# Kernel optimization log

Measured on AMD Instinct MI355X. Metric: run time of the kernel, lower is better.

The kernel has to match this reference:

```python
import jax, jax.numpy as jnp
import numpy as np

NQ = 4096
N0, N1 = 32768, 8192
N = N0 + N1
F = 128          # emb_dim (32x0e+32x1e)
H = 4            # num_heads
HD = F // H
NB = 64          # fc_neurons[0] radial basis size
DEG = 32
CUTOFFS = jnp.array([2.0, 4.0], dtype=jnp.float32)
OFFSETS = jnp.array([0.1, 0.2], dtype=jnp.float32)


def _sph_harm(u):
    # component-normalized real spherical harmonics l=0,1,2 of unit vectors u [E,3]
    x, y, z = u[:, 0], u[:, 1], u[:, 2]
    s3, s15, s5 = 3.0 ** 0.5, 15.0 ** 0.5, 5.0 ** 0.5
    return jnp.stack([
        jnp.ones_like(x),
        s3 * x, s3 * y, s3 * z,
        s15 * x * y, s15 * y * z, 0.5 * s5 * (3.0 * z * z - 1.0),
        s15 * x * z, 0.5 * s15 * (x * x - y * y),
    ], axis=-1)  # [E,9]


def setup_inputs() -> dict:
    key = jax.random.key(0)
    ks = jax.random.split(key, 20)
    E0 = NQ * DEG
    E1 = NQ * DEG
    edge_src = jnp.concatenate([
        jax.random.randint(ks[0], (E0,), 0, N0),
        jax.random.randint(ks[1], (E1,), N0, N),
    ])
    edge_dst = jnp.concatenate([
        jax.random.randint(ks[2], (E0,), 0, NQ),
        jax.random.randint(ks[3], (E1,), 0, NQ),
    ])
    scale_id = jnp.concatenate([jnp.zeros((E0,), jnp.int32), jnp.ones((E1,), jnp.int32)])
    r = lambda k, sh, s=1.0: jax.random.normal(k, sh, jnp.float32) * s
    return {
        'query_coord': r(ks[4], (NQ, 3)),
        'node_feature': r(ks[5], (N, F)),
        'node_coord': r(ks[6], (N, 3)),
        'edge_src': edge_src, 'edge_dst': edge_dst, 'scale_id': scale_id,
        'b_dst': r(ks[7], (F,)),
        'Wq': r(ks[8], (F, F), F ** -0.5),
        'Wk': r(ks[9], (F, F), F ** -0.5),
        'Wv': r(ks[10], (F, F), F ** -0.5),
        'Wo': r(ks[11], (F, F), F ** -0.5),
        'bo': r(ks[12], (F,)),
        'W_rad0': r(ks[13], (NB, NB), NB ** -0.5), 'b_rad0': r(ks[14], (NB,)),
        'W_rad1': r(ks[15], (NB, NB), NB ** -0.5), 'b_rad1': r(ks[16], (NB,)),
        'W_msg': r(ks[17], (NB, F), NB ** -0.5),
        'W_sh': r(ks[18], (9, F), 9 ** -0.5),
        'W_alpha': r(ks[19], (NB, H), NB ** -0.5),
    }


def _forward(query_coord, node_feature, node_coord, b_dst, Wq, Wk, Wv, Wo, bo,
             W_rad0, b_rad0, W_rad1, b_rad1, W_msg, W_sh, W_alpha,
             edge_src, edge_dst, scale_id):
    Nq = query_coord.shape[0]
    vec = node_coord[edge_src] - query_coord[edge_dst]            # [E,3]
    rlen = jnp.sqrt(jnp.sum(vec * vec, -1) + 1e-12)               # [E]
    off = OFFSETS[scale_id]
    cut = CUTOFFS[scale_id]
    xn = (rlen - off) / (cut - off)                               # normalized radius per scale
    centers = jnp.linspace(0.0, 1.0, NB)
    std = 1.0 / NB
    g = jnp.exp(-0.5 * ((xn[:, None] - centers) / std) ** 2)      # [E,NB] gaussian RBF
    soft = 0.5 * (1.0 + jnp.cos(jnp.pi * jnp.clip((xn - 0.8) / 0.2, 0.0, 1.0)))
    g = g * soft[:, None]                                         # soft finite cutoff
    # per-scale Linear after radial basis (2 scales, masked select)
    edge_scalar = jnp.where((scale_id == 0)[:, None], g @ W_rad0 + b_rad0, g @ W_rad1 + b_rad1)
    sh = _sph_harm(vec / rlen[:, None])                           # [E,9]
    # attention GNN (equiformer-style): dst features start as zeros + learned bias
    q = (b_dst @ Wq).reshape(H, HD)
    k = (node_feature @ Wk)[edge_src].reshape(-1, H, HD)
    logits = jnp.einsum('hd,ehd->eh', q, k) / (HD ** 0.5) + edge_scalar @ W_alpha  # [E,H]
    m = jax.ops.segment_max(logits, edge_dst, num_segments=Nq)
    p = jnp.exp(logits - m[edge_dst])
    denom = jax.ops.segment_sum(p, edge_dst, num_segments=Nq)
    alpha = p / (denom[edge_dst] + 1e-9)                          # segment softmax [E,H]
    v_e = (node_feature @ Wv)[edge_src] * (edge_scalar @ W_msg) + sh @ W_sh  # [E,F]
    msg = (alpha[:, :, None] * v_e.reshape(-1, H, HD)).reshape(-1, F)
    out = jax.ops.segment_sum(msg, edge_dst, num_segments=Nq)     # [Nq,F]
    return out @ Wo + bo


def reference(query_coord, node_feature, node_coord, edge_src, edge_dst, scale_id,
              b_dst, Wq, Wk, Wv, Wo, bo, W_rad0, b_rad0, W_rad1, b_rad1,
              W_msg, W_sh, W_alpha):
    return _forward(query_coord, node_feature, node_coord, b_dst, Wq, Wk, Wv, Wo, bo,
                    W_rad0, b_rad0, W_rad1, b_rad1, W_msg, W_sh, W_alpha,
                    edge_src, edge_dst, scale_id)
```

## Files before the change

### kernel.cpp

```cpp
#include <hip/hip_runtime.h>
#include <hip/hip_bf16.h>
#include <math.h>

#define PI_F 3.14159265358979323846f

typedef __attribute__((ext_vector_type(8))) short short8v;
typedef __attribute__((ext_vector_type(4))) float f32x4;

__device__ __forceinline__ short f2bf(float x) {
    return __builtin_bit_cast(short, __float2bfloat16(x));
}
__device__ __forceinline__ float bf2f(unsigned short u) {
    return __uint_as_float(((unsigned)u) << 16);
}
__device__ __forceinline__ int pack_bf2(float a, float b) {
    return (int)(unsigned short)f2bf(a) | ((int)(unsigned short)f2bf(b) << 16);
}

static const size_t WS_WA     = 0;
static const size_t WS_BA     = 512;
static const size_t WS_BM     = 520;
static const size_t WS_WMF    = 776;
static const size_t WS_WSHF   = 8968;
static const size_t WS_QKF    = 11016;
static const size_t WS_WVF    = 12040;
static const size_t WS_WOF    = 20232;
static const size_t WS_COUNTS = 28424;
static const size_t WS_OFFS   = 36624;
static const size_t WS_CURSOR = 44824;
static const size_t WS_PACKED = 53016;
static const size_t WS_LK     = 315160;
static const size_t WS_EDP    = 479000;
static const size_t WS_EDG    = 1527576;
static const size_t WS_VB     = 2576152;
static const size_t WS_OUTPRE = 5197592;

__global__ __launch_bounds__(256) void k_prepfmt(
    const float* b_dst, const float* Wq, const float* Wk,
    const float* W_rad0, const float* b_rad0,
    const float* W_rad1, const float* b_rad1,
    const float* W_msg, const float* W_alpha, const float* Wv,
    const float* Wo, const float* W_sh,
    float* Wa, float* ba, float* bm,
    short* WmF, short* WshF, short* QKF, short* WVF, short* WOF,
    int* counts, int nkey) {
    __shared__ float qs_s[128];
    __shared__ float qk_s[512];
    int t = threadIdx.x;
    int b = blockIdx.x;
    if (b == 0) {
        if (t < 128) {
            float acc = 0.f;
            for (int c = 0; c < 128; ++c) acc += b_dst[c] * Wq[c * 128 + t];
            qs_s[t] = acc;
        }
        __syncthreads();
        if (t < 128) {
            const float invs = 0.17677669529663687f;
            for (int h = 0; h < 4; ++h) {
                float acc = 0.f;
                for (int d = 0; d < 32; ++d)
                    acc += Wk[t * 128 + h * 32 + d] * qs_s[h * 32 + d];
                qk_s[t * 4 + h] = acc * invs;
            }
        }
        for (int idx = t; idx < 512; idx += 256) {
            int s = idx >> 8, i = (idx >> 2) & 63, h = idx & 3;
            const float* Wr = s ? W_rad1 : W_rad0;
            float acc = 0.f;
            for (int u = 0; u < 64; ++u) acc += Wr[i * 64 + u] * W_alpha[u * 4 + h];
            Wa[idx] = acc;
        }
        if (t < 8) {
            int s = t >> 2, h = t & 3;
            const float* br = s ? b_rad1 : b_rad0;
            float acc = 0.f;
            for (int u = 0; u < 64; ++u) acc += br[u] * W_alpha[u * 4 + h];
            ba[t] = acc;
        }
        {
            int s = t >> 7, c = t & 127;
            const float* br = s ? b_rad1 : b_rad0;
            float acc = 0.f;
            for (int u = 0; u < 64; ++u) acc += br[u] * W_msg[u * 128 + c];
            bm[t] = acc;
        }
        __syncthreads();
        for (int idx = t; idx < 2048; idx += 256) {
            int j = idx & 7, lane = (idx >> 3) & 63, kh = idx >> 9;
            int k = kh * 32 + ((lane >> 4) << 3) + j;
            int col = lane & 15;
            QKF[idx] = f2bf(col < 4 ? qk_s[k * 4 + col] : 0.f);
        }
    } else if (b <= 208) {
        int item = (b - 1) * 256 + t;
        if (item < 16384) {
            int j = item & 7, lane = (item >> 3) & 63, kh = (item >> 9) & 1;
            int ct = (item >> 10) & 7, sid = item >> 13;
            int k = kh * 32 + ((lane >> 4) << 3) + j;
            int c = (lane & 15) * 8 + ct;
            const float* Wr = sid ? W_rad1 : W_rad0;
            float acc = 0.f;
            for (int u = 0; u < 64; ++u) acc += Wr[k * 64 + u] * W_msg[u * 128 + c];
            WmF[item] = f2bf(acc);
        } else if (item < 20480) {
            int i2 = item - 16384;
            int j = i2 & 7, lane = (i2 >> 3) & 63, ct = (i2 >> 9) & 7;
            int k = ((lane >> 4) << 3) + j;
            int c = (lane & 15) * 8 + ct;
            WshF[i2] = f2bf(k < 9 ? W_sh[k * 128 + c] : 0.f);
        } else if (item < 36864) {
            int i2 = item - 20480;
            int j = i2 & 7, lane = (i2 >> 3) & 63, ct = (i2 >> 9) & 7, kh = (i2 >> 12) & 3;
            int k = kh * 32 + ((lane >> 4) << 3) + j;
            int c = (lane & 15) * 8 + ct;
            WVF[i2] = f2bf(Wv[k * 128 + c]);
        } else {
            int i2 = item - 36864;
            int j = i2 & 7, lane = (i2 >> 3) & 63, ct = (i2 >> 9) & 7, kh = (i2 >> 12) & 3;
            int k = kh * 32 + ((lane >> 4) << 3) + j;
            int c = (lane & 15) * 8 + ct;
            WOF[i2] = f2bf(Wo[k * 128 + c]);
        }
    } else {
        int idx = (b - 209) * 256 + t;
        if (idx < nkey) counts[idx] = 0;
    }
}

template <typename OUT, bool LK>
__global__ __launch_bounds__(256) void k_mgemm(
    const float* A, const short* WF, const float* bias, OUT* out,
    float* lk, const short* QKF, int M,
    const int* edge_dst, const int* scale_id, int* counts, int E, int NQr) {
    int gb = (M + 63) >> 6;
    if ((int)blockIdx.x >= gb) {
        int e = ((int)blockIdx.x - gb) * 256 + (int)threadIdx.x;
        if (e < E) atomicAdd(&counts[scale_id[e] * NQr + edge_dst[e]], 1);
        return;
    }
    int t = threadIdx.x;
    int w = t >> 6, lane = t & 63;
    int m = lane & 15, grp = lane >> 4;
    int row0 = (blockIdx.x * 4 + w) * 16;
    if (row0 >= M) return;

    short8v a[4];
#pragma unroll
    for (int kh = 0; kh < 4; ++kh) {
        const float* ap = &A[(size_t)(row0 + m) * 128 + kh * 32 + grp * 8];
        float4 f0 = *(const float4*)ap;
        float4 f1 = *(const float4*)(ap + 4);
        a[kh][0] = f2bf(f0.x); a[kh][1] = f2bf(f0.y);
        a[kh][2] = f2bf(f0.z); a[kh][3] = f2bf(f0.w);
        a[kh][4] = f2bf(f1.x); a[kh][5] = f2bf(f1.y);
        a[kh][6] = f2bf(f1.z); a[kh][7] = f2bf(f1.w);
    }
    if constexpr (LK) {
        f32x4 cl = {0.f, 0.f, 0.f, 0.f};
#pragma unroll
        for (int kh = 0; kh < 4; ++kh) {
            short8v qb = *(const short8v*)&QKF[(kh * 64 + lane) * 8];
            cl = __builtin_amdgcn_mfma_f32_16x16x32_bf16(a[kh], qb, cl, 0, 0, 0);
        }
        if (m < 4) {
#pragma unroll
            for (int r = 0; r < 4; ++r)
                lk[(size_t)(row0 + grp * 4 + r) * 4 + m] = cl[r];
        }
    }
    f32x4 c8[8];
#pragma unroll
    for (int ct = 0; ct < 8; ++ct) {
        f32x4 c = {0.f, 0.f, 0.f, 0.f};
#pragma unroll
        for (int kh = 0; kh < 4; ++kh) {
            short8v bf = *(const short8v*)&WF[((kh * 8 + ct) * 64 + lane) * 8];
            c = __builtin_amdgcn_mfma_f32_16x16x32_bf16(a[kh], bf, c, 0, 0, 0);
        }
        c8[ct] = c;
    }
    if constexpr (sizeof(OUT) == 2) {
#pragma unroll
        for (int r = 0; r < 4; ++r) {
            int row = row0 + grp * 4 + r;
            int4 sv;
            sv.x = pack_bf2(c8[0][r], c8[1][r]);
            sv.y = pack_bf2(c8[2][r], c8[3][r]);
            sv.z = pack_bf2(c8[4][r], c8[5][r]);
            sv.w = pack_bf2(c8[6][r], c8[7][r]);
            *(int4*)&out[(size_t)row * 128 + m * 8] = sv;
        }
    } else {
        float4 b0 = make_float4(0.f, 0.f, 0.f, 0.f), b1 = b0;
        if (bias) {
            b0 = *(const float4*)&bias[m * 8];
            b1 = *(const float4*)&bias[m * 8 + 4];
        }
#pragma unroll
        for (int r = 0; r < 4; ++r) {
            int row = row0 + grp * 4 + r;
            float4 o0 = make_float4(c8[0][r] + b0.x, c8[1][r] + b0.y,
                                    c8[2][r] + b0.z, c8[3][r] + b0.w);
            float4 o1 = make_float4(c8[4][r] + b1.x, c8[5][r] + b1.y,
                                    c8[6][r] + b1.z, c8[7][r] + b1.w);
            *(float4*)&out[(size_t)row * 128 + m * 8] = o0;
            *(float4*)&out[(size_t)row * 128 + m * 8 + 4] = o1;
        }
    }
}

__global__ void k_scan(const int* counts, int* offsets, int* cursor, int nkey) {
    __shared__ int sdata[256];
    int t = threadIdx.x;
    int chunk = (nkey + 255) / 256;
    int sum = 0;
    for (int i = 0; i < chunk; ++i) {
        int idx = t * chunk + i;
        sum += (idx < nkey) ? counts[idx] : 0;
    }
    sdata[t] = sum;
    __syncthreads();
    for (int off = 1; off < 256; off <<= 1) {
        int v = (t >= off) ? sdata[t - off] : 0;
        __syncthreads();
        sdata[t] += v;
        __syncthreads();
    }
    int run = sdata[t] - sum;
    for (int i = 0; i < chunk; ++i) {
        int idx = t * chunk + i;
        if (idx < nkey) {
            offsets[idx] = run;
            cursor[idx] = run;
            run += counts[idx];
        }
    }
    if (t == 255) offsets[nkey] = sdata[255];
}

__global__ __launch_bounds__(256) void k_scatter_edge(
    const int* edge_src, const int* edge_dst, const int* scale_id,
    const float* qc, const float* nc, const float* lk,
    const float* WaB, const float* baB, int* cursor,
    int* packed, float* edP, float* edG, int E, int NQr) {
    __shared__ float WaS[512];
    __shared__ float baS[8];
    int t = threadIdx.x;
    for (int i = t; i < 512; i += 256) WaS[i] = WaB[i];
    if (t < 8) baS[t] = baB[t];
    __syncthreads();
    int e = blockIdx.x * 256 + t;
    if (e >= E) return;
    int src = edge_src[e], dst = edge_dst[e], sid = scale_id[e];
    int pos = atomicAdd(&cursor[sid * NQr + dst], 1);

    float qx = qc[dst * 3 + 0], qy = qc[dst * 3 + 1], qz = qc[dst * 3 + 2];
    float vx = nc[src * 3 + 0] - qx;
    float vy = nc[src * 3 + 1] - qy;
    float vz = nc[src * 3 + 2] - qz;
    float r = sqrtf(vx * vx + vy * vy + vz * vz + 1e-12f);
    float rinv = 1.0f / r;
    float ux = vx * rinv, uy = vy * rinv, uz = vz * rinv;

    float roff = sid ? 0.2f : 0.1f;
    float rdiv = sid ? (1.0f / 3.8f) : (1.0f / 1.9f);
    float xn = (r - roff) * rdiv;
    float su = fminf(fmaxf((xn - 0.8f) * 5.0f, 0.0f), 1.0f);
    float soft = 0.5f * (1.0f + __cosf(PI_F * su));

    float4 lkv = *(const float4*)&lk[(size_t)src * 4];

    const float qs = 64.f / 63.f;
    const float Qc = __expf(-qs * qs);
    const float* Wrow = WaS + sid * 256;
    float a0 = 0.f, a1 = 0.f, a2 = 0.f, a3 = 0.f;
#pragma unroll
    for (int ch = 0; ch < 8; ++ch) {
        float d = (xn - (float)(ch * 8) * (1.0f / 63.0f)) * 64.0f;
        float g = __expf(-0.5f * d * d);
        float tt = __expf(fminf(qs * d - 0.5f * qs * qs, 60.f));
#pragma unroll
        for (int j = 0; j < 8; ++j) {
            float4 wa = *(const float4*)&Wrow[(ch * 8 + j) * 4];
            a0 = fmaf(g, wa.x, a0);
            a1 = fmaf(g, wa.y, a1);
            a2 = fmaf(g, wa.z, a2);
            a3 = fmaf(g, wa.w, a3);
            g *= tt; tt *= Qc;
        }
    }
    float p0 = __expf(lkv.x + soft * a0 + baS[sid * 4 + 0]);
    float p1 = __expf(lkv.y + soft * a1 + baS[sid * 4 + 1]);
    float p2 = __expf(lkv.z + soft * a2 + baS[sid * 4 + 2]);
    float p3 = __expf(lkv.w + soft * a3 + baS[sid * 4 + 3]);
    packed[pos] = src | (dst << 16);
    *(float4*)&edP[(size_t)pos * 4] = make_float4(p0, p1, p2, p3);
    *(float4*)&edG[(size_t)pos * 4] = make_float4(ux, uy, uz, xn);
}

__device__ __forceinline__ short8v gchain(float xn, int k0, float soft, float Qc) {
    const float qs = 64.f / 63.f;
    float d = (xn - (float)k0 * (1.0f / 63.0f)) * 64.0f;
    float g = __expf(-0.5f * d * d);
    float tt = __expf(fminf(qs * d - 0.5f * qs * qs, 60.f));
    short8v rr;
#pragma unroll
    for (int j = 0; j < 8; ++j) {
        rr[j] = f2bf(g * soft);
        g *= tt; tt *= Qc;
    }
    return rr;
}

__global__ __launch_bounds__(256) void k_main10(
    const int* offsets, const int* packed, const float* edP, const float* edG,
    const unsigned short* Vu, const float* bm, const short* WmF, const short* WshF,
    float* out_pre, int NQr) {
    __shared__ float part[4][132];
    int t = threadIdx.x;
    int w = t >> 6, lane = t & 63;
    int sid = w & 1;
    int dst = blockIdx.x * 2 + (w >> 1);
    int m = lane & 15, grp = lane >> 4;
    int h = m >> 2;

    int key = sid * NQr + dst;
    int s0 = offsets[key], s1 = offsets[key + 1];
    int nt = (s1 - s0 + 15) >> 4;

    float acc[8];
#pragma unroll
    for (int i = 0; i < 8; ++i) acc[i] = 0.f;
    float den = 0.f;

    float4 bm0 = *(const float4*)&bm[sid * 128 + m * 8];
    float4 bm1 = *(const float4*)&bm[sid * 128 + m * 8 + 4];
    float bmv[8] = {bm0.x, bm0.y, bm0.z, bm0.w, bm1.x, bm1.y, bm1.z, bm1.w};
    const short* wmp = WmF + sid * 8192;

    const float qs = 64.f / 63.f;
    const float Qc = __expf(-qs * qs);
    const float s3 = 1.7320508075688772f, s15 = 3.872983346207417f, s5 = 2.23606797749979f;

    if (nt > 0) {
        auto loadA = [&](int tl, int (&srcs)[4], float (&ph)[4], float4& G4) {
            int q0 = s0 + tl * 16;
            int posA = q0 + m; if (posA >= s1) posA = s1 - 1;
            G4 = *(const float4*)&edG[(size_t)posA * 4];
#pragma unroll
            for (int r = 0; r < 4; ++r) {
                int pos = q0 + grp * 4 + r;
                bool valid = pos < s1;
                if (!valid) pos = s1 - 1;
                srcs[r] = packed[pos] & 0xFFFF;
                float p = edP[(size_t)pos * 4 + h];
                ph[r] = valid ? p : 0.f;
            }
        };
        auto loadV = [&](const int (&srcs)[4], int4 (&vv)[4]) {
#pragma unroll
            for (int r = 0; r < 4; ++r)
                vv[r] = *(const int4*)&Vu[(size_t)srcs[r] * 128 + m * 8];
        };

        int srcsA[4], srcsB[4], srcsC[4];
        float phA[4], phB[4], phC[4];
        float4 gA, gB, gC;
        int4 vA[4], vB[4];

        loadA(0, srcsA, phA, gA);
        loadV(srcsA, vA);
        if (nt > 1) loadA(1, srcsB, phB, gB);

        for (int tl = 0; tl < nt; ++tl) {
            if (tl + 1 < nt) loadV(srcsB, vB);
            if (tl + 2 < nt) loadA(tl + 2, srcsC, phC, gC);

            int wds[4][4];
#pragma unroll
            for (int r = 0; r < 4; ++r) {
                wds[r][0] = vA[r].x; wds[r][1] = vA[r].y;
                wds[r][2] = vA[r].z; wds[r][3] = vA[r].w;
            }
            den += phA[0] + phA[1] + phA[2] + phA[3];

            float xn = gA.w;
            float su = fminf(fmaxf((xn - 0.8f) * 5.0f, 0.0f), 1.0f);
            float soft = 0.5f * (1.0f + __cosf(PI_F * su));
            short8v aG0 = gchain(xn, grp * 8, soft, Qc);
            short8v aG1 = gchain(xn, 32 + grp * 8, soft, Qc);

            float ux = gA.x, uy = gA.y, uz = gA.z;
            float sh[9];
            sh[0] = 1.f; sh[1] = s3 * ux; sh[2] = s3 * uy; sh[3] = s3 * uz;
            sh[4] = s15 * ux * uy; sh[5] = s15 * uy * uz;
            sh[6] = 0.5f * s5 * (3.f * uz * uz - 1.f);
            sh[7] = s15 * ux * uz; sh[8] = 0.5f * s15 * (ux * ux - uy * uy);
            short8v aS;
#pragma unroll
            for (int j = 0; j < 8; ++j) {
                float v = (grp == 0) ? sh[j] : ((grp == 1 && j == 0) ? sh[8] : 0.f);
                aS[j] = f2bf(v);
            }

#pragma unroll
            for (int ct = 0; ct < 8; ++ct) {
                short8v b0 = *(const short8v*)&wmp[((ct * 2 + 0) * 64 + lane) * 8];
                short8v b1 = *(const short8v*)&wmp[((ct * 2 + 1) * 64 + lane) * 8];
                short8v bS = *(const short8v*)&WshF[(ct * 64 + lane) * 8];
                f32x4 cms = {bmv[ct], bmv[ct], bmv[ct], bmv[ct]};
                cms = __builtin_amdgcn_mfma_f32_16x16x32_bf16(aG0, b0, cms, 0, 0, 0);
                cms = __builtin_amdgcn_mfma_f32_16x16x32_bf16(aG1, b1, cms, 0, 0, 0);
                f32x4 csh = {0.f, 0.f, 0.f, 0.f};
                csh = __builtin_amdgcn_mfma_f32_16x16x32_bf16(aS, bS, csh, 0, 0, 0);
#pragma unroll
                for (int r = 0; r < 4; ++r) {
                    int wd = wds[r][ct >> 1];
                    unsigned short vu = (ct & 1) ? (unsigned short)(wd >> 16)
                                                 : (unsigned short)(wd & 0xFFFF);
                    float vf = bf2f(vu);
                    float ve = fmaf(vf, cms[r], csh[r]);
                    acc[ct] = fmaf(phA[r], ve, acc[ct]);
                }
            }

            gA = gB; gB = gC;
#pragma unroll
            for (int r = 0; r < 4; ++r) {
                phA[r] = phB[r]; phB[r] = phC[r];
                srcsB[r] = srcsC[r];
                vA[r] = vB[r];
            }
        }
    }

#pragma unroll
    for (int i = 0; i < 8; ++i) {
        acc[i] += __shfl_xor(acc[i], 16);
        acc[i] += __shfl_xor(acc[i], 32);
    }
    den += __shfl_xor(den, 16);
    den += __shfl_xor(den, 32);
    if (lane < 16) {
#pragma unroll
        for (int ct = 0; ct < 8; ++ct) part[w][m * 8 + ct] = acc[ct];
        if ((m & 3) == 0) part[w][128 + h] = den;
    }
    __syncthreads();

    {
        int which = t >> 7;
        int col = t & 127;
        int d2 = blockIdx.x * 2 + which;
        if (d2 < NQr) {
            int hh = col >> 5;
            float s = part[2 * which][col] + part[2 * which + 1][col];
            float d = part[2 * which][128 + hh] + part[2 * which + 1][128 + hh];
            out_pre[(size_t)d2 * 128 + col] = s / (d + 1e-9f);
        }
    }
}

extern "C" void kernel_launch(void* const* d_in, const int* in_sizes, int n_in,
                              void* d_out, int out_size, void* d_ws, size_t ws_size,
                              hipStream_t stream) {
    const float* query_coord = (const float*)d_in[0];
    const float* node_feature = (const float*)d_in[1];
    const float* node_coord = (const float*)d_in[2];
    const int* edge_src = (const int*)d_in[3];
    const int* edge_dst = (const int*)d_in[4];
    const int* scale_id = (const int*)d_in[5];
    const float* b_dst = (const float*)d_in[6];
    const float* Wq = (const float*)d_in[7];
    const float* Wk = (const float*)d_in[8];
    const float* Wv = (const float*)d_in[9];
    const float* Wo = (const float*)d_in[10];
    const float* bo = (const float*)d_in[11];
    const float* W_rad0 = (const float*)d_in[12];
    const float* b_rad0 = (const float*)d_in[13];
    const float* W_rad1 = (const float*)d_in[14];
    const float* b_rad1 = (const float*)d_in[15];
    const float* W_msg = (const float*)d_in[16];
    const float* W_sh = (const float*)d_in[17];
    const float* W_alpha = (const float*)d_in[18];
    (void)n_in; (void)ws_size; (void)out_size;

    int NQr = in_sizes[0] / 3;
    int Nn = in_sizes[1] / 128;
    int E = in_sizes[3];
    int nkey = NQr * 2;

    float* ws = (float*)d_ws;
    float* Wa = ws + WS_WA;
    float* ba = ws + WS_BA;
    float* bm = ws + WS_BM;
    short* WmF = (short*)(ws + WS_WMF);
    short* WshF = (short*)(ws + WS_WSHF);
    short* QKF = (short*)(ws + WS_QKF);
    short* WVF = (short*)(ws + WS_WVF);
    short* WOF = (short*)(ws + WS_WOF);
    int* counts = (int*)(ws + WS_COUNTS);
    int* offsets = (int*)(ws + WS_OFFS);
    int* cursor = (int*)(ws + WS_CURSOR);
    int* packed = (int*)(ws + WS_PACKED);
    float* lk = ws + WS_LK;
    float* edP = ws + WS_EDP;
    float* edG = ws + WS_EDG;
    unsigned short* Vb = (unsigned short*)(ws + WS_VB);
    float* out_pre = ws + WS_OUTPRE;
    float* out = (float*)d_out;

    int zeroBlocks = (nkey + 255) / 256;
    int histBlocks = (E + 255) / 256;
    int gemmVBlocks = (Nn + 63) / 64;
    hipLaunchKernelGGL(k_prepfmt, dim3(209 + zeroBlocks), dim3(256), 0, stream,
                       b_dst, Wq, Wk, W_rad0, b_rad0, W_rad1, b_rad1, W_msg, W_alpha,
                       Wv, Wo, W_sh, Wa, ba, bm, WmF, WshF, QKF, WVF, WOF, counts, nkey);
    hipLaunchKernelGGL((k_mgemm<unsigned short, true>), dim3(gemmVBlocks + histBlocks),
                       dim3(256), 0, stream,
                       node_feature, WVF, (const float*)nullptr, Vb, lk, QKF, Nn,
                       edge_dst, scale_id, counts, E, NQr);
    hipLaunchKernelGGL(k_scan, dim3(1), dim3(256), 0, stream, counts, offsets, cursor, nkey);
    hipLaunchKernelGGL(k_scatter_edge, dim3((E + 255) / 256), dim3(256), 0, stream,
                       edge_src, edge_dst, scale_id, query_coord, node_coord, lk,
                       Wa, ba, cursor, packed, edP, edG, E, NQr);
    hipLaunchKernelGGL(k_main10, dim3((NQr + 1) / 2), dim3(256), 0, stream,
                       offsets, packed, edP, edG, Vb, bm, WmF, WshF, out_pre, NQr);
    hipLaunchKernelGGL((k_mgemm<float, false>), dim3((NQr + 63) / 64), dim3(256), 0, stream,
                       out_pre, WOF, bo, out, (float*)nullptr, (const short*)nullptr, NQr,
                       (const int*)nullptr, (const int*)nullptr, (int*)nullptr, 0, 0);
}
```

Baseline: 124.0 us.

## Schedule segment waves by descending tile count and fuse normalization into output GEMM

The scan kernel now also counting-sorts the (scale, dst) keys by number of 16-edge tiles in descending order. The main kernel assigns one key per wavefront from this sorted list, so long segments start first and wave lengths are balanced. Per-scale partial sums and denominators are written separately, and the combine-plus-divide moves into the output GEMM's A-load. This drops the shared-memory reduction and block barrier in the main kernel, at the cost of a longer single-block scan and extra partial-buffer traffic.

```diff
diff --git a/kernel.cpp b/kernel.cpp
--- a/kernel.cpp
+++ b/kernel.cpp
@@ -3,6 +3,7 @@
 #include <math.h>
 
 #define PI_F 3.14159265358979323846f
+#define NBIN 2048
 
 typedef __attribute__((ext_vector_type(8))) short short8v;
 typedef __attribute__((ext_vector_type(4))) float f32x4;
@@ -33,7 +34,9 @@
 static const size_t WS_EDP    = 479000;
 static const size_t WS_EDG    = 1527576;
 static const size_t WS_VB     = 2576152;
-static const size_t WS_OUTPRE = 5197592;
+static const size_t WS_SORT   = 5197592;
+static const size_t WS_OPART  = 5205784;
+static const size_t WS_DPART  = 6254360;
 
 __global__ __launch_bounds__(256) void k_prepfmt(
     const float* b_dst, const float* Wq, const float* Wk,
@@ -128,16 +131,18 @@
     }
 }
 
-template <typename OUT, bool LK>
+template <typename OUT, int MODE>
 __global__ __launch_bounds__(256) void k_mgemm(
-    const float* A, const short* WF, const float* bias, OUT* out,
+    const float* A, const float* den, const short* WF, const float* bias, OUT* out,
     float* lk, const short* QKF, int M,
     const int* edge_dst, const int* scale_id, int* counts, int E, int NQr) {
     int gb = (M + 63) >> 6;
-    if ((int)blockIdx.x >= gb) {
-        int e = ((int)blockIdx.x - gb) * 256 + (int)threadIdx.x;
-        if (e < E) atomicAdd(&counts[scale_id[e] * NQr + edge_dst[e]], 1);
-        return;
+    if constexpr (MODE == 1) {
+        if ((int)blockIdx.x >= gb) {
+            int e = ((int)blockIdx.x - gb) * 256 + (int)threadIdx.x;
+            if (e < E) atomicAdd(&counts[scale_id[e] * NQr + edge_dst[e]], 1);
+            return;
+        }
     }
     int t = threadIdx.x;
     int w = t >> 6, lane = t & 63;
@@ -146,17 +151,39 @@
     if (row0 >= M) return;
 
     short8v a[4];
-#pragma unroll
-    for (int kh = 0; kh < 4; ++kh) {
-        const float* ap = &A[(size_t)(row0 + m) * 128 + kh * 32 + grp * 8];
-        float4 f0 = *(const float4*)ap;
-        float4 f1 = *(const float4*)(ap + 4);
-        a[kh][0] = f2bf(f0.x); a[kh][1] = f2bf(f0.y);
-        a[kh][2] = f2bf(f0.z); a[kh][3] = f2bf(f0.w);
-        a[kh][4] = f2bf(f1.x); a[kh][5] = f2bf(f1.y);
-        a[kh][6] = f2bf(f1.z); a[kh][7] = f2bf(f1.w);
-    }
-    if constexpr (LK) {
+    if constexpr (MODE == 2) {
+        int row = row0 + m;
+        float4 d0 = *(const float4*)&den[(size_t)row * 4];
+        float4 d1 = *(const float4*)&den[(size_t)(M + row) * 4];
+        float dinv[4] = {1.f / (d0.x + d1.x + 1e-9f), 1.f / (d0.y + d1.y + 1e-9f),
+                         1.f / (d0.z + d1.z + 1e-9f), 1.f / (d0.w + d1.w + 1e-9f)};
+#pragma unroll
+        for (int kh = 0; kh < 4; ++kh) {
+            const float* apA = &A[(size_t)row * 128 + kh * 32 + grp * 8];
+            const float* apB = &A[(size_t)(M + row) * 128 + kh * 32 + grp * 8];
+            float4 fa0 = *(const float4*)apA;
+            float4 fa1 = *(const float4*)(apA + 4);
+            float4 fb0 = *(const float4*)apB;
+            float4 fb1 = *(const float4*)(apB + 4);
+            float s = dinv[kh];
+            a[kh][0] = f2bf((fa0.x + fb0.x) * s); a[kh][1] = f2bf((fa0.y + fb0.y) * s);
+            a[kh][2] = f2bf((fa0.z + fb0.z) * s); a[kh][3] = f2bf((fa0.w + fb0.w) * s);
+            a[kh][4] = f2bf((fa1.x + fb1.x) * s); a[kh][5] = f2bf((fa1.y + fb1.y) * s);
+            a[kh][6] = f2bf((fa1.z + fb1.z) * s); a[kh][7] = f2bf((fa1.w + fb1.w) * s);
+        }
+    } else {
+#pragma unroll
+        for (int kh = 0; kh < 4; ++kh) {
+            const float* ap = &A[(size_t)(row0 + m) * 128 + kh * 32 + grp * 8];
+            float4 f0 = *(const float4*)ap;
+            float4 f1 = *(const float4*)(ap + 4);
+            a[kh][0] = f2bf(f0.x); a[kh][1] = f2bf(f0.y);
+            a[kh][2] = f2bf(f0.z); a[kh][3] = f2bf(f0.w);
+            a[kh][4] = f2bf(f1.x); a[kh][5] = f2bf(f1.y);
+            a[kh][6] = f2bf(f1.z); a[kh][7] = f2bf(f1.w);
+        }
+    }
+    if constexpr (MODE == 1) {
         f32x4 cl = {0.f, 0.f, 0.f, 0.f};
 #pragma unroll
         for (int kh = 0; kh < 4; ++kh) {
@@ -210,8 +237,11 @@
     }
 }
 
-__global__ void k_scan(const int* counts, int* offsets, int* cursor, int nkey) {
+__global__ void k_scan(const int* counts, int* offsets, int* cursor,
+                       int* sortedKeys, int nkey) {
     __shared__ int sdata[256];
+    __shared__ int hbin[NBIN];
+    __shared__ int hstart[NBIN];
     int t = threadIdx.x;
     int chunk = (nkey + 255) / 256;
     int sum = 0;
@@ -237,6 +267,54 @@
         }
     }
     if (t == 255) offsets[nkey] = sdata[255];
+    __syncthreads();
+
+    for (int i = t; i < NBIN; i += 256) hbin[i] = 0;
+    __syncthreads();
+    for (int i = 0; i < chunk; ++i) {
+        int idx = t * chunk + i;
+        if (idx < nkey) {
+            int nt = (counts[idx] + 15) >> 4;
+            if (nt > NBIN - 1) nt = NBIN - 1;
+            atomicAdd(&hbin[nt], 1);
+        }
+    }
+    __syncthreads();
+    {
+        int local = 0;
+#pragma unroll
+        for (int j = 0; j < NBIN / 256; ++j) local += hbin[t * (NBIN / 256) + j];
+        sdata[t] = local;
+        __syncthreads();
+        for (int off = 1; off < 256; off <<= 1) {
+            int v = (t >= off) ? sdata[t - off] : 0;
+            __syncthreads();
+            sdata[t] += v;
+            __syncthreads();
+        }
+        int total = sdata[255];
+        int before = sdata[t] - local;
+        int run2 = before;
+#pragma unroll
+        for (int j = 0; j < NBIN / 256; ++j) {
+            int bb = t * (NBIN / 256) + j;
+            int c = hbin[bb];
+            hstart[bb] = total - run2 - c;
+            run2 += c;
+        }
+    }
+    __syncthreads();
+    for (int i = t; i < NBIN; i += 256) hbin[i] = hstart[i];
+    __syncthreads();
+    for (int i = 0; i < chunk; ++i) {
+        int idx = t * chunk + i;
+        if (idx < nkey) {
+            int nt = (counts[idx] + 15) >> 4;
+            if (nt > NBIN - 1) nt = NBIN - 1;
+            int slot = atomicAdd(&hbin[nt], 1);
+            sortedKeys[slot] = idx;
+        }
+    }
 }
 
 __global__ __launch_bounds__(256) void k_scatter_edge(
@@ -313,19 +391,18 @@
     return rr;
 }
 
-__global__ __launch_bounds__(256) void k_main10(
+__global__ __launch_bounds__(256) void k_main12(
     const int* offsets, const int* packed, const float* edP, const float* edG,
     const unsigned short* Vu, const float* bm, const short* WmF, const short* WshF,
-    float* out_pre, int NQr) {
-    __shared__ float part[4][132];
+    const int* sortedKeys, float* out_part, float* den_part, int NQr) {
     int t = threadIdx.x;
     int w = t >> 6, lane = t & 63;
-    int sid = w & 1;
-    int dst = blockIdx.x * 2 + (w >> 1);
+    int slot = blockIdx.x * 4 + w;
+    int key = sortedKeys[slot];
+    int sid = (key >= NQr) ? 1 : 0;
     int m = lane & 15, grp = lane >> 4;
     int h = m >> 2;
 
-    int key = sid * NQr + dst;
     int s0 = offsets[key], s1 = offsets[key + 1];
     int nt = (s1 - s0 + 15) >> 4;
 
@@ -443,22 +520,11 @@
     den += __shfl_xor(den, 16);
     den += __shfl_xor(den, 32);
     if (lane < 16) {
-#pragma unroll
-        for (int ct = 0; ct < 8; ++ct) part[w][m * 8 + ct] = acc[ct];
-        if ((m & 3) == 0) part[w][128 + h] = den;
-    }
-    __syncthreads();
-
-    {
-        int which = t >> 7;
-        int col = t & 127;
-        int d2 = blockIdx.x * 2 + which;
-        if (d2 < NQr) {
-            int hh = col >> 5;
-            float s = part[2 * which][col] + part[2 * which + 1][col];
-            float d = part[2 * which][128 + hh] + part[2 * which + 1][128 + hh];
-            out_pre[(size_t)d2 * 128 + col] = s / (d + 1e-9f);
-        }
+        float4 o0 = make_float4(acc[0], acc[1], acc[2], acc[3]);
+        float4 o1 = make_float4(acc[4], acc[5], acc[6], acc[7]);
+        *(float4*)&out_part[(size_t)key * 128 + m * 8] = o0;
+        *(float4*)&out_part[(size_t)key * 128 + m * 8 + 4] = o1;
+        if ((m & 3) == 0) den_part[(size_t)key * 4 + h] = den;
     }
 }
 
@@ -508,7 +574,9 @@
     float* edP = ws + WS_EDP;
     float* edG = ws + WS_EDG;
     unsigned short* Vb = (unsigned short*)(ws + WS_VB);
-    float* out_pre = ws + WS_OUTPRE;
+    int* sortedKeys = (int*)(ws + WS_SORT);
+    float* out_part = ws + WS_OPART;
+    float* den_part = ws + WS_DPART;
     float* out = (float*)d_out;
 
     int zeroBlocks = (nkey + 255) / 256;
@@ -517,17 +585,20 @@
     hipLaunchKernelGGL(k_prepfmt, dim3(209 + zeroBlocks), dim3(256), 0, stream,
                        b_dst, Wq, Wk, W_rad0, b_rad0, W_rad1, b_rad1, W_msg, W_alpha,
                        Wv, Wo, W_sh, Wa, ba, bm, WmF, WshF, QKF, WVF, WOF, counts, nkey);
-    hipLaunchKernelGGL((k_mgemm<unsigned short, true>), dim3(gemmVBlocks + histBlocks),
+    hipLaunchKernelGGL((k_mgemm<unsigned short, 1>), dim3(gemmVBlocks + histBlocks),
                        dim3(256), 0, stream,
-                       node_feature, WVF, (const float*)nullptr, Vb, lk, QKF, Nn,
-                       edge_dst, scale_id, counts, E, NQr);
-    hipLaunchKernelGGL(k_scan, dim3(1), dim3(256), 0, stream, counts, offsets, cursor, nkey);
+                       node_feature, (const float*)nullptr, WVF, (const float*)nullptr,
+                       Vb, lk, QKF, Nn, edge_dst, scale_id, counts, E, NQr);
+    hipLaunchKernelGGL(k_scan, dim3(1), dim3(256), 0, stream,
+                       counts, offsets, cursor, sortedKeys, nkey);
     hipLaunchKernelGGL(k_scatter_edge, dim3((E + 255) / 256), dim3(256), 0, stream,
                        edge_src, edge_dst, scale_id, query_coord, node_coord, lk,
                        Wa, ba, cursor, packed, edP, edG, E, NQr);
-    hipLaunchKernelGGL(k_main10, dim3((NQr + 1) / 2), dim3(256), 0, stream,
-                       offsets, packed, edP, edG, Vb, bm, WmF, WshF, out_pre, NQr);
-    hipLaunchKernelGGL((k_mgemm<float, false>), dim3((NQr + 63) / 64), dim3(256), 0, stream,
-                       out_pre, WOF, bo, out, (float*)nullptr, (const short*)nullptr, NQr,
+    hipLaunchKernelGGL(k_main12, dim3(nkey / 4), dim3(256), 0, stream,
+                       offsets, packed, edP, edG, Vb, bm, WmF, WshF,
+                       sortedKeys, out_part, den_part, NQr);
+    hipLaunchKernelGGL((k_mgemm<float, 2>), dim3((NQr + 63) / 64), dim3(256), 0, stream,
+                       out_part, den_part, WOF, bo, out,
+                       (float*)nullptr, (const short*)nullptr, NQr,
                        (const int*)nullptr, (const int*)nullptr, (int*)nullptr, 0, 0);
 }
```

Result: slower. 137.8 us (+11.1%).

## Fuse output projection Wo into main aggregation kernel epilogue

Applied to the files above, without the earlier changes.

The final Wo projection plus bias moves into the epilogue of the main per-query aggregation kernel. Each block normalizes its two query rows into shared memory, then runs a scalar FP32 FMA loop over the 128x128 Wo read from global memory. This drops a kernel launch, the out_pre round trip through memory, and the bf16 conversion of Wo in the prep kernel. In exchange, every block re-reads all of Wo (likely served from cache) and does the GEMM without MFMA, and the d2 < NQr bounds check is gone.

```diff
diff --git a/kernel.cpp b/kernel.cpp
--- a/kernel.cpp
+++ b/kernel.cpp
@@ -24,7 +24,6 @@
 static const size_t WS_WSHF   = 8968;
 static const size_t WS_QKF    = 11016;
 static const size_t WS_WVF    = 12040;
-static const size_t WS_WOF    = 20232;
 static const size_t WS_COUNTS = 28424;
 static const size_t WS_OFFS   = 36624;
 static const size_t WS_CURSOR = 44824;
@@ -33,16 +32,15 @@
 static const size_t WS_EDP    = 479000;
 static const size_t WS_EDG    = 1527576;
 static const size_t WS_VB     = 2576152;
-static const size_t WS_OUTPRE = 5197592;
 
 __global__ __launch_bounds__(256) void k_prepfmt(
     const float* b_dst, const float* Wq, const float* Wk,
     const float* W_rad0, const float* b_rad0,
     const float* W_rad1, const float* b_rad1,
     const float* W_msg, const float* W_alpha, const float* Wv,
-    const float* Wo, const float* W_sh,
+    const float* W_sh,
     float* Wa, float* ba, float* bm,
-    short* WmF, short* WshF, short* QKF, short* WVF, short* WOF,
+    short* WmF, short* WshF, short* QKF, short* WVF,
     int* counts, int nkey) {
     __shared__ float qs_s[128];
     __shared__ float qk_s[512];
@@ -92,7 +90,7 @@
             int col = lane & 15;
             QKF[idx] = f2bf(col < 4 ? qk_s[k * 4 + col] : 0.f);
         }
-    } else if (b <= 208) {
+    } else if (b <= 144) {
         int item = (b - 1) * 256 + t;
         if (item < 16384) {
             int j = item & 7, lane = (item >> 3) & 63, kh = (item >> 9) & 1;
@@ -109,28 +107,21 @@
             int k = ((lane >> 4) << 3) + j;
             int c = (lane & 15) * 8 + ct;
             WshF[i2] = f2bf(k < 9 ? W_sh[k * 128 + c] : 0.f);
-        } else if (item < 36864) {
+        } else {
             int i2 = item - 20480;
             int j = i2 & 7, lane = (i2 >> 3) & 63, ct = (i2 >> 9) & 7, kh = (i2 >> 12) & 3;
             int k = kh * 32 + ((lane >> 4) << 3) + j;
             int c = (lane & 15) * 8 + ct;
             WVF[i2] = f2bf(Wv[k * 128 + c]);
-        } else {
-            int i2 = item - 36864;
-            int j = i2 & 7, lane = (i2 >> 3) & 63, ct = (i2 >> 9) & 7, kh = (i2 >> 12) & 3;
-            int k = kh * 32 + ((lane >> 4) << 3) + j;
-            int c = (lane & 15) * 8 + ct;
-            WOF[i2] = f2bf(Wo[k * 128 + c]);
         }
     } else {
-        int idx = (b - 209) * 256 + t;
+        int idx = (b - 145) * 256 + t;
         if (idx < nkey) counts[idx] = 0;
     }
 }
 
-template <typename OUT, bool LK>
-__global__ __launch_bounds__(256) void k_mgemm(
-    const float* A, const short* WF, const float* bias, OUT* out,
+__global__ __launch_bounds__(256) void k_mgemmV(
+    const float* A, const short* WF, unsigned short* out,
     float* lk, const short* QKF, int M,
     const int* edge_dst, const int* scale_id, int* counts, int E, int NQr) {
     int gb = (M + 63) >> 6;
@@ -156,7 +147,7 @@
         a[kh][4] = f2bf(f1.x); a[kh][5] = f2bf(f1.y);
         a[kh][6] = f2bf(f1.z); a[kh][7] = f2bf(f1.w);
     }
-    if constexpr (LK) {
+    {
         f32x4 cl = {0.f, 0.f, 0.f, 0.f};
 #pragma unroll
         for (int kh = 0; kh < 4; ++kh) {
@@ -180,33 +171,15 @@
         }
         c8[ct] = c;
     }
-    if constexpr (sizeof(OUT) == 2) {
-#pragma unroll
-        for (int r = 0; r < 4; ++r) {
-            int row = row0 + grp * 4 + r;
-            int4 sv;
-            sv.x = pack_bf2(c8[0][r], c8[1][r]);
-            sv.y = pack_bf2(c8[2][r], c8[3][r]);
-            sv.z = pack_bf2(c8[4][r], c8[5][r]);
-            sv.w = pack_bf2(c8[6][r], c8[7][r]);
-            *(int4*)&out[(size_t)row * 128 + m * 8] = sv;
-        }
-    } else {
-        float4 b0 = make_float4(0.f, 0.f, 0.f, 0.f), b1 = b0;
-        if (bias) {
-            b0 = *(const float4*)&bias[m * 8];
-            b1 = *(const float4*)&bias[m * 8 + 4];
-        }
-#pragma unroll
-        for (int r = 0; r < 4; ++r) {
-            int row = row0 + grp * 4 + r;
-            float4 o0 = make_float4(c8[0][r] + b0.x, c8[1][r] + b0.y,
-                                    c8[2][r] + b0.z, c8[3][r] + b0.w);
-            float4 o1 = make_float4(c8[4][r] + b1.x, c8[5][r] + b1.y,
-                                    c8[6][r] + b1.z, c8[7][r] + b1.w);
-            *(float4*)&out[(size_t)row * 128 + m * 8] = o0;
-            *(float4*)&out[(size_t)row * 128 + m * 8 + 4] = o1;
-        }
+#pragma unroll
+    for (int r = 0; r < 4; ++r) {
+        int row = row0 + grp * 4 + r;
+        int4 sv;
+        sv.x = pack_bf2(c8[0][r], c8[1][r]);
+        sv.y = pack_bf2(c8[2][r], c8[3][r]);
+        sv.z = pack_bf2(c8[4][r], c8[5][r]);
+        sv.w = pack_bf2(c8[6][r], c8[7][r]);
+        *(int4*)&out[(size_t)row * 128 + m * 8] = sv;
     }
 }
 
@@ -313,11 +286,12 @@
     return rr;
 }
 
-__global__ __launch_bounds__(256) void k_main10(
+__global__ __launch_bounds__(256) void k_main13(
     const int* offsets, const int* packed, const float* edP, const float* edG,
     const unsigned short* Vu, const float* bm, const short* WmF, const short* WshF,
-    float* out_pre, int NQr) {
+    const float* Wo, const float* bo, float* out, int NQr) {
     __shared__ float part[4][132];
+    __shared__ float preS[2][128];
     int t = threadIdx.x;
     int w = t >> 6, lane = t & 63;
     int sid = w & 1;
@@ -449,16 +423,23 @@
     }
     __syncthreads();
 
+    int which = t >> 7;
+    int col = t & 127;
     {
-        int which = t >> 7;
-        int col = t & 127;
+        int hh = col >> 5;
+        float s = part[2 * which][col] + part[2 * which + 1][col];
+        float d = part[2 * which][128 + hh] + part[2 * which + 1][128 + hh];
+        preS[which][col] = s / (d + 1e-9f);
+    }
+    __syncthreads();
+
+    {
         int d2 = blockIdx.x * 2 + which;
-        if (d2 < NQr) {
-            int hh = col >> 5;
-            float s = part[2 * which][col] + part[2 * which + 1][col];
-            float d = part[2 * which][128 + hh] + part[2 * which + 1][128 + hh];
-            out_pre[(size_t)d2 * 128 + col] = s / (d + 1e-9f);
-        }
+        float oacc = bo[col];
+#pragma unroll 4
+        for (int k = 0; k < 128; ++k)
+            oacc = fmaf(preS[which][k], Wo[k * 128 + col], oacc);
+        out[(size_t)d2 * 128 + col] = oacc;
     }
 }
 
@@ -499,7 +480,6 @@
     short* WshF = (short*)(ws + WS_WSHF);
     short* QKF = (short*)(ws + WS_QKF);
     short* WVF = (short*)(ws + WS_WVF);
-    short* WOF = (short*)(ws + WS_WOF);
     int* counts = (int*)(ws + WS_COUNTS);
     int* offsets = (int*)(ws + WS_OFFS);
     int* cursor = (int*)(ws + WS_CURSOR);
@@ -508,26 +488,22 @@
     float* edP = ws + WS_EDP;
     float* edG = ws + WS_EDG;
     unsigned short* Vb = (unsigned short*)(ws + WS_VB);
-    float* out_pre = ws + WS_OUTPRE;
     float* out = (float*)d_out;
 
     int zeroBlocks = (nkey + 255) / 256;
     int histBlocks = (E + 255) / 256;
     int gemmVBlocks = (Nn + 63) / 64;
-    hipLaunchKernelGGL(k_prepfmt, dim3(209 + zeroBlocks), dim3(256), 0, stream,
+    hipLaunchKernelGGL(k_prepfmt, dim3(145 + zeroBlocks), dim3(256), 0, stream,
                        b_dst, Wq, Wk, W_rad0, b_rad0, W_rad1, b_rad1, W_msg, W_alpha,
-                       Wv, Wo, W_sh, Wa, ba, bm, WmF, WshF, QKF, WVF, WOF, counts, nkey);
-    hipLaunchKernelGGL((k_mgemm<unsigned short, true>), dim3(gemmVBlocks + histBlocks),
-                       dim3(256), 0, stream,
-                       node_feature, WVF, (const float*)nullptr, Vb, lk, QKF, Nn,
+                       Wv, W_sh, Wa, ba, bm, WmF, WshF, QKF, WVF, counts, nkey);
+    hipLaunchKernelGGL(k_mgemmV, dim3(gemmVBlocks + histBlocks), dim3(256), 0, stream,
+                       node_feature, WVF, Vb, lk, QKF, Nn,
                        edge_dst, scale_id, counts, E, NQr);
     hipLaunchKernelGGL(k_scan, dim3(1), dim3(256), 0, stream, counts, offsets, cursor, nkey);
     hipLaunchKernelGGL(k_scatter_edge, dim3((E + 255) / 256), dim3(256), 0, stream,
                        edge_src, edge_dst, scale_id, query_coord, node_coord, lk,
                        Wa, ba, cursor, packed, edP, edG, E, NQr);
-    hipLaunchKernelGGL(k_main10, dim3((NQr + 1) / 2), dim3(256), 0, stream,
-                       offsets, packed, edP, edG, Vb, bm, WmF, WshF, out_pre, NQr);
-    hipLaunchKernelGGL((k_mgemm<float, false>), dim3((NQr + 63) / 64), dim3(256), 0, stream,
-                       out_pre, WOF, bo, out, (float*)nullptr, (const short*)nullptr, NQr,
-                       (const int*)nullptr, (const int*)nullptr, (int*)nullptr, 0, 0);
-}
+    hipLaunchKernelGGL(k_main13, dim3((NQr + 1) / 2), dim3(256), 0, stream,
+                       offsets, packed, edP, edG, Vb, bm, WmF, WshF,
+                       Wo, bo, out, NQr);
+}
```

Measured after the change: 137.9 us. 11.1% more time.

## Schedule main kernel destinations in descending work order via counting sort

Applied to the files above, without the earlier changes.

Adds a counting sort inside the single-block scan kernel that orders destination nodes by their tile count (edges per scale in groups of 16), largest first. The main aggregation kernel then reads its destination index from this sorted list so heavy destinations are dispatched first, which targets load imbalance and tail effects. It costs extra serial work in the one-block scan kernel and an indirection read. With NQr odd, the removed bounds check could touch an invalid entry, though NQ is even here.

```diff
diff --git a/kernel.cpp b/kernel.cpp
--- a/kernel.cpp
+++ b/kernel.cpp
@@ -3,6 +3,7 @@
 #include <math.h>
 
 #define PI_F 3.14159265358979323846f
+#define NBIN 2048
 
 typedef __attribute__((ext_vector_type(8))) short short8v;
 typedef __attribute__((ext_vector_type(4))) float f32x4;
@@ -34,6 +35,7 @@
 static const size_t WS_EDG    = 1527576;
 static const size_t WS_VB     = 2576152;
 static const size_t WS_OUTPRE = 5197592;
+static const size_t WS_SORTD  = 5721880;
 
 __global__ __launch_bounds__(256) void k_prepfmt(
     const float* b_dst, const float* Wq, const float* Wk,
@@ -210,8 +212,11 @@
     }
 }
 
-__global__ void k_scan(const int* counts, int* offsets, int* cursor, int nkey) {
+__global__ void k_scan(const int* counts, int* offsets, int* cursor,
+                       int* sortedDst, int nkey, int NQr) {
     __shared__ int sdata[256];
+    __shared__ int hbin[NBIN];
+    __shared__ int hstart[NBIN];
     int t = threadIdx.x;
     int chunk = (nkey + 255) / 256;
     int sum = 0;
@@ -237,6 +242,55 @@
         }
     }
     if (t == 255) offsets[nkey] = sdata[255];
+    __syncthreads();
+
+    for (int i = t; i < NBIN; i += 256) hbin[i] = 0;
+    __syncthreads();
+    int chunkD = (NQr + 255) / 256;
+    for (int i = 0; i < chunkD; ++i) {
+        int d = t * chunkD + i;
+        if (d < NQr) {
+            int nt = ((counts[d] + 15) >> 4) + ((counts[NQr + d] + 15) >> 4);
+            if (nt > NBIN - 1) nt = NBIN - 1;
+            atomicAdd(&hbin[nt], 1);
+        }
+    }
+    __syncthreads();
+    {
+        int local = 0;
+#pragma unroll
+        for (int j = 0; j < NBIN / 256; ++j) local += hbin[t * (NBIN / 256) + j];
+        sdata[t] = local;
+        __syncthreads();
+        for (int off = 1; off < 256; off <<= 1) {
+            int v = (t >= off) ? sdata[t - off] : 0;
+            __syncthreads();
+            sdata[t] += v;
+            __syncthreads();
+        }
+        int total = sdata[255];
+        int before = sdata[t] - local;
+        int run2 = before;
+#pragma unroll
+        for (int j = 0; j < NBIN / 256; ++j) {
+            int bb = t * (NBIN / 256) + j;
+            int c = hbin[bb];
+            hstart[bb] = total - run2 - c;
+            run2 += c;
+        }
+    }
+    __syncthreads();
+    for (int i = t; i < NBIN; i += 256) hbin[i] = hstart[i];
+    __syncthreads();
+    for (int i = 0; i < chunkD; ++i) {
+        int d = t * chunkD + i;
+        if (d < NQr) {
+            int nt = ((counts[d] + 15) >> 4) + ((counts[NQr + d] + 15) >> 4);
+            if (nt > NBIN - 1) nt = NBIN - 1;
+            int slot = atomicAdd(&hbin[nt], 1);
+            sortedDst[slot] = d;
+        }
+    }
 }
 
 __global__ __launch_bounds__(256) void k_scatter_edge(
@@ -316,12 +370,12 @@
 __global__ __launch_bounds__(256) void k_main10(
     const int* offsets, const int* packed, const float* edP, const float* edG,
     const unsigned short* Vu, const float* bm, const short* WmF, const short* WshF,
-    float* out_pre, int NQr) {
+    const int* sortedDst, float* out_pre, int NQr) {
     __shared__ float part[4][132];
     int t = threadIdx.x;
     int w = t >> 6, lane = t & 63;
     int sid = w & 1;
-    int dst = blockIdx.x * 2 + (w >> 1);
+    int dst = sortedDst[blockIdx.x * 2 + (w >> 1)];
     int m = lane & 15, grp = lane >> 4;
     int h = m >> 2;
 
@@ -452,13 +506,11 @@
     {
         int which = t >> 7;
         int col = t & 127;
-        int d2 = blockIdx.x * 2 + which;
-        if (d2 < NQr) {
-            int hh = col >> 5;
-            float s = part[2 * which][col] + part[2 * which + 1][col];
-            float d = part[2 * which][128 + hh] + part[2 * which + 1][128 + hh];
-            out_pre[(size_t)d2 * 128 + col] = s / (d + 1e-9f);
-        }
+        int d2 = sortedDst[blockIdx.x * 2 + which];
+        int hh = col >> 5;
+        float s = part[2 * which][col] + part[2 * which + 1][col];
+        float d = part[2 * which][128 + hh] + part[2 * which + 1][128 + hh];
+        out_pre[(size_t)d2 * 128 + col] = s / (d + 1e-9f);
     }
 }
 
@@ -509,6 +561,7 @@
     float* edG = ws + WS_EDG;
     unsigned short* Vb = (unsigned short*)(ws + WS_VB);
     float* out_pre = ws + WS_OUTPRE;
+    int* sortedDst = (int*)(ws + WS_SORTD);
     float* out = (float*)d_out;
 
     int zeroBlocks = (nkey + 255) / 256;
@@ -521,12 +574,14 @@
                        dim3(256), 0, stream,
                        node_feature, WVF, (const float*)nullptr, Vb, lk, QKF, Nn,
                        edge_dst, scale_id, counts, E, NQr);
-    hipLaunchKernelGGL(k_scan, dim3(1), dim3(256), 0, stream, counts, offsets, cursor, nkey);
+    hipLaunchKernelGGL(k_scan, dim3(1), dim3(256), 0, stream,
+                       counts, offsets, cursor, sortedDst, nkey, NQr);
     hipLaunchKernelGGL(k_scatter_edge, dim3((E + 255) / 256), dim3(256), 0, stream,
                        edge_src, edge_dst, scale_id, query_coord, node_coord, lk,
                        Wa, ba, cursor, packed, edP, edG, E, NQr);
     hipLaunchKernelGGL(k_main10, dim3((NQr + 1) / 2), dim3(256), 0, stream,
-                       offsets, packed, edP, edG, Vb, bm, WmF, WshF, out_pre, NQr);
+                       offsets, packed, edP, edG, Vb, bm, WmF, WshF,
+                       sortedDst, out_pre, NQr);
     hipLaunchKernelGGL((k_mgemm<float, false>), dim3((NQr + 63) / 64), dim3(256), 0, stream,
                        out_pre, WOF, bo, out, (float*)nullptr, (const short*)nullptr, NQr,
                        (const int*)nullptr, (const int*)nullptr, (int*)nullptr, 0, 0);
```

After: 132.3 us. 6.7% more time.
